# Optimization experiments

Measured on AMD Instinct MI355X. Metric: run time of the kernel, lower is better.

## Reference

```python
import jax, jax.numpy as jnp
import numpy as np

N, D, E, K = 16384, 512, 8, 2  # tokens, model dim, experts, top_k


def setup_inputs() -> dict:
    key = jax.random.key(0)
    k_x, k_l, k_w = jax.random.split(key, 3)
    input_batch = jax.random.normal(k_x, (N, D), dtype=jnp.float32)
    # Router-like top-k gates: distinct expert ids per token (matches the
    # module's assumption that each (token, slot) maps to a unique expert row).
    logits = jax.random.normal(k_l, (N, E), dtype=jnp.float32)
    top_vals, top_idx = jax.lax.top_k(logits, K)
    probabilities = jax.nn.softmax(top_vals, axis=-1)          # [N, K]
    indices = top_idx.astype(jnp.int32)                        # [N, K]
    W = jax.random.normal(k_w, (E, D, D), dtype=jnp.float32) * (1.0 / np.sqrt(D))
    b = jnp.zeros((E, D), dtype=jnp.float32)
    return {"input_batch": input_batch, "probabilities": probabilities,
            "indices": indices, "W": W, "b": b}


def reference(input_batch, probabilities, indices, W, b):
    # Original loops over experts, gathers tokens routed to each expert,
    # runs the expert, concatenates, restores original (token, slot) order,
    # applies AFTER_EXPERTS gate weighting, and sums over the top_k slots.
    # Equivalent vectorized math: out[n] = sum_k p[n,k] * expert_{idx[n,k]}(x[n]).
    y = jnp.einsum('nd,edo->eno', input_batch, W) + b[:, None, :]   # [E, N, D]
    n_ar = jnp.arange(input_batch.shape[0])[:, None]                # [N, 1]
    gathered = y[indices, n_ar]                                     # [N, K, D]
    output = jnp.sum(probabilities[..., None] * gathered, axis=1)   # [N, D]
    total_loss = jnp.float32(0.0)  # sampler_loss=0 (external indices), expert losses=0
    return output, total_loss
```

## Files before the change

kernel.cpp:

```cpp
#include <hip/hip_runtime.h>

#define NTOK 16384
#define DIM  512
#define NEXP 8
#define NPAIR 64
#define PCAP 8192

#define BM 128
#define BN 64
#define BK 32

typedef __bf16 bf16x8 __attribute__((ext_vector_type(8)));
typedef __bf16 bf16x4 __attribute__((ext_vector_type(4)));
typedef float  f32x4  __attribute__((ext_vector_type(4)));

__device__ __forceinline__ void async_cp16(const void* g, void* l) {
    __builtin_amdgcn_global_load_lds((const __attribute__((address_space(1))) void*)g,
                                     (__attribute__((address_space(3))) void*)l, 16, 0, 0);
}

__global__ __launch_bounds__(256) void k_prep(const float* __restrict__ W,
                                              __bf16* __restrict__ Wt,
                                              const float* __restrict__ x,
                                              __bf16* __restrict__ xb,
                                              const int* __restrict__ indices,
                                              const float* __restrict__ probs,
                                              int* __restrict__ cnt,
                                              int* __restrict__ tok_arr,
                                              float* __restrict__ plo_arr,
                                              float* __restrict__ phi_arr,
                                              float* __restrict__ out) {
    int b = blockIdx.x, tid = threadIdx.x;
    if (b < 2048) {
        __shared__ __bf16 tile[32][34];
        int e = b >> 8, rem = b & 255;
        int o0 = (rem >> 4) * 32, k0 = (rem & 15) * 32;
        const float* Wsrc = W + ((size_t)e * DIM + k0) * DIM + o0;
        for (int i = tid; i < 1024; i += 256) {
            int kk = i >> 5, oo = i & 31;
            tile[oo][kk] = (__bf16)Wsrc[(size_t)kk * DIM + oo];
        }
        __syncthreads();
        __bf16* dst = Wt + ((size_t)(e * 16 + (k0 >> 5)) * DIM + o0) * 32;
        for (int i = tid; i < 1024; i += 256) {
            int oo = i >> 5, kk = i & 31;
            dst[oo * 32 + kk] = tile[oo][kk];
        }
    } else if (b < 2304) {
        int base = (b - 2048) * 256 + tid;
        const float4* src = (const float4*)x;
        #pragma unroll
        for (int it = 0; it < 32; ++it) {
            int i = base + it * 65536;
            float4 v = src[i];
            bf16x4 h; h[0] = (__bf16)v.x; h[1] = (__bf16)v.y; h[2] = (__bf16)v.z; h[3] = (__bf16)v.w;
            *(bf16x4*)&xb[(size_t)i * 4] = h;
        }
    } else {
        __shared__ int lcnt[NPAIR], lbase[NPAIR];
        int t = (b - 2304) * 256 + tid;
        if (tid < NPAIR) lcnt[tid] = 0;
        __syncthreads();
        int   e0 = indices[2 * t], e1 = indices[2 * t + 1];
        float p0 = probs[2 * t],   p1 = probs[2 * t + 1];
        int lo = min(e0, e1), hi = max(e0, e1);
        float plo = (e0 < e1) ? p0 : p1;
        float phi = (e0 < e1) ? p1 : p0;
        int key = lo * 8 + hi;
        int lr = atomicAdd(&lcnt[key], 1);
        __syncthreads();
        if (tid < NPAIR) lbase[tid] = atomicAdd(&cnt[tid], lcnt[tid]);
        __syncthreads();
        int pos = lbase[key] + lr;
        if (pos < PCAP) {
            int q = key * PCAP + pos;
            tok_arr[q] = t; plo_arr[q] = plo; phi_arr[q] = phi;
        }
        if (b == 2304 && tid == 0) out[NTOK * DIM] = 0.0f;
    }
}

__global__ __launch_bounds__(256) void k_gemm(const __bf16* __restrict__ xb,
                                              const __bf16* __restrict__ Wt,
                                              const float* __restrict__ bias,
                                              const int* __restrict__ tok_arr,
                                              const float* __restrict__ plo_arr,
                                              const float* __restrict__ phi_arr,
                                              const int* __restrict__ cnt,
                                              float* __restrict__ out) {
    int p = blockIdx.x;
    int r = p & 7;
    int nt = (p >> 3) & 7;
    int m_slot = (p >> 6) * 8 + r;
    int key = -1, m_t = 0, count = 0, total = 0;
    for (int i = 0; i < NPAIR; ++i) {
        int c = cnt[i];
        int tl = (c + BM - 1) >> 7;
        if (key < 0 && m_slot < total + tl) { key = i; m_t = m_slot - total; count = c; }
        total += tl;
    }
    if (key < 0) return;
    if (count > PCAP) count = PCAP;
    int lo = key >> 3, hi = key & 7;
    int m0 = m_t * BM, n0 = nt * BN, tid = threadIdx.x;

    __shared__ __attribute__((aligned(16))) char smem[32768];
    __shared__ int   sTok[BM];
    __shared__ float sPlo[BM], sPhi[BM];

    if (tid < BM) {
        int g = m0 + tid;
        int tk = 0; float a = 0.f, h = 0.f;
        if (g < count) {
            int q = key * PCAP + g;
            tk = tok_arr[q]; a = plo_arr[q]; h = phi_arr[q];
        }
        sTok[tid] = tk;
        sPlo[tid] = a; sPhi[tid] = h;
    }
    __syncthreads();

    int wid  = tid >> 6, lane = tid & 63;
    int quad = lane >> 4, rr  = lane & 15;
    int wm = (wid >> 1) * 64, wn = (wid & 1) * 32;

    int rA0 = tid >> 2;
    int swz = ((tid & 3) ^ (rA0 & 3)) << 3;
    const __bf16* gA0 = xb + (size_t)sTok[rA0]      * DIM + swz;
    const __bf16* gA1 = xb + (size_t)sTok[rA0 + 64] * DIM + swz;
    size_t bOff = (size_t)((rA0 * 4 + ((tid & 3) ^ (rA0 & 3))) * 8);
    const __bf16* gBlo = Wt + ((size_t)(lo * 16) * DIM + n0) * 32 + bOff;
    const __bf16* gBhi = Wt + ((size_t)(hi * 16) * DIM + n0) * 32 + bOff;

    f32x4 accL[4][2] = {};
    f32x4 accH[4][2] = {};

    async_cp16(gA0,  smem + tid * 16);
    async_cp16(gA1,  smem + tid * 16 + 4096);
    async_cp16(gBlo, smem + 16384 + tid * 16);
    async_cp16(gBhi, smem + 24576 + tid * 16);

    #pragma unroll 2
    for (int kt = 0; kt < 16; ++kt) {
        int cur = kt & 1;
        __syncthreads();
        if (kt < 15) {
            int ka = (kt + 1) * BK;
            size_t wOff = (size_t)(kt + 1) * DIM * 32;
            int nx = (kt + 1) & 1;
            async_cp16(gA0 + ka,    smem + nx * 8192 + tid * 16);
            async_cp16(gA1 + ka,    smem + nx * 8192 + tid * 16 + 4096);
            async_cp16(gBlo + wOff, smem + 16384 + nx * 4096 + tid * 16);
            async_cp16(gBhi + wOff, smem + 24576 + nx * 4096 + tid * 16);
        }
        const __bf16* sA  = (const __bf16*)(smem +         cur * 8192);
        const __bf16* sBl = (const __bf16*)(smem + 16384 + cur * 4096);
        const __bf16* sBh = (const __bf16*)(smem + 24576 + cur * 4096);
        int csw = (quad ^ (rr & 3)) * 8;
        bf16x8 af[4], bl[2], bh[2];
        #pragma unroll
        for (int i = 0; i < 4; ++i)
            af[i] = *(bf16x8*)&sA[(wm + i * 16 + rr) * BK + csw];
        #pragma unroll
        for (int j = 0; j < 2; ++j) {
            bl[j] = *(bf16x8*)&sBl[(wn + j * 16 + rr) * BK + csw];
            bh[j] = *(bf16x8*)&sBh[(wn + j * 16 + rr) * BK + csw];
        }
        #pragma unroll
        for (int i = 0; i < 4; ++i)
            #pragma unroll
            for (int j = 0; j < 2; ++j) {
                accL[i][j] = __builtin_amdgcn_mfma_f32_16x16x32_bf16(af[i], bl[j], accL[i][j], 0, 0, 0);
                accH[i][j] = __builtin_amdgcn_mfma_f32_16x16x32_bf16(af[i], bh[j], accH[i][j], 0, 0, 0);
            }
    }

    float blo[2], bhi[2];
    #pragma unroll
    for (int j = 0; j < 2; ++j) {
        blo[j] = bias[lo * DIM + n0 + wn + j * 16 + rr];
        bhi[j] = bias[hi * DIM + n0 + wn + j * 16 + rr];
    }
    #pragma unroll
    for (int i = 0; i < 4; ++i) {
        #pragma unroll
        for (int reg = 0; reg < 4; ++reg) {
            int row = wm + i * 16 + quad * 4 + reg;
            int g = m0 + row;
            if (g >= count) continue;
            int   tk = sTok[row];
            float pl = sPlo[row], ph = sPhi[row];
            float* dst = out + (size_t)tk * DIM + n0 + wn + rr;
            #pragma unroll
            for (int j = 0; j < 2; ++j)
                dst[j * 16] = accL[i][j][reg] * pl + accH[i][j][reg] * ph + pl * blo[j] + ph * bhi[j];
        }
    }
}

extern "C" void kernel_launch(void* const* d_in, const int* in_sizes, int n_in,
                              void* d_out, int out_size, void* d_ws, size_t ws_size,
                              hipStream_t stream) {
    const float* x    = (const float*)d_in[0];
    const float* prob = (const float*)d_in[1];
    const int*   idx  = (const int*)d_in[2];
    const float* W    = (const float*)d_in[3];
    const float* b    = (const float*)d_in[4];
    float* out = (float*)d_out;

    char* ws = (char*)d_ws;
    __bf16* Wt      = (__bf16*)ws;
    __bf16* xb      = (__bf16*)(ws + 4194304);
    int*    cnt     = (int*)   (ws + 4194304 + 16777216);
    int*    tok_arr = (int*)   (ws + 4194304 + 16777216 + 256);
    float*  plo_arr = (float*) (ws + 4194304 + 16777216 + 256 + 2097152);
    float*  phi_arr = (float*) (ws + 4194304 + 16777216 + 256 + 2 * 2097152);

    (void)hipMemsetAsync(cnt, 0, NPAIR * sizeof(int), stream);
    hipLaunchKernelGGL(k_prep, dim3(2368), dim3(256), 0, stream,
                       W, Wt, x, xb, idx, prob, cnt, tok_arr, plo_arr, phi_arr, out);
    hipLaunchKernelGGL(k_gemm, dim3(1280), dim3(256), 0, stream,
                       xb, Wt, b, tok_arr, plo_arr, phi_arr, cnt, out);
}
```

Before: 138.1 us.

## Triple-buffer GEMM LDS with explicit vmcnt waits and MFMA priority

Switches the grouped expert GEMM from double to triple buffering in LDS, so loads are issued two k-steps ahead. The combined syncthreads is replaced by explicit s_waitcnt vmcnt plus s_barrier, and the loop is fully unrolled. The MFMA block is wrapped in s_setprio, and launch bounds ask for 3 blocks per CU. The goal is to hide global-load latency behind compute, at the cost of 48KB LDS per block, which may limit occupancy, and of fragile manual vmcnt accounting.

Measured after the change: 137.4 us. No clear change (-0.5%).

```diff
diff --git a/kernel.cpp b/kernel.cpp
--- a/kernel.cpp
+++ b/kernel.cpp
@@ -80,14 +80,14 @@
     }
 }
 
-__global__ __launch_bounds__(256) void k_gemm(const __bf16* __restrict__ xb,
-                                              const __bf16* __restrict__ Wt,
-                                              const float* __restrict__ bias,
-                                              const int* __restrict__ tok_arr,
-                                              const float* __restrict__ plo_arr,
-                                              const float* __restrict__ phi_arr,
-                                              const int* __restrict__ cnt,
-                                              float* __restrict__ out) {
+__global__ __launch_bounds__(256, 3) void k_gemm(const __bf16* __restrict__ xb,
+                                                 const __bf16* __restrict__ Wt,
+                                                 const float* __restrict__ bias,
+                                                 const int* __restrict__ tok_arr,
+                                                 const float* __restrict__ plo_arr,
+                                                 const float* __restrict__ phi_arr,
+                                                 const int* __restrict__ cnt,
+                                                 float* __restrict__ out) {
     int p = blockIdx.x;
     int r = p & 7;
     int nt = (p >> 3) & 7;
@@ -104,7 +104,7 @@
     int lo = key >> 3, hi = key & 7;
     int m0 = m_t * BM, n0 = nt * BN, tid = threadIdx.x;
 
-    __shared__ __attribute__((aligned(16))) char smem[32768];
+    __shared__ __attribute__((aligned(16))) char smem[49152];
     __shared__ int   sTok[BM];
     __shared__ float sPlo[BM], sPhi[BM];
 
@@ -135,27 +135,30 @@
     f32x4 accL[4][2] = {};
     f32x4 accH[4][2] = {};
 
-    async_cp16(gA0,  smem + tid * 16);
-    async_cp16(gA1,  smem + tid * 16 + 4096);
-    async_cp16(gBlo, smem + 16384 + tid * 16);
-    async_cp16(gBhi, smem + 24576 + tid * 16);
-
-    #pragma unroll 2
+    auto issue = [&](int kt, int b) {
+        int ka = kt * BK;
+        size_t wOff = (size_t)kt * DIM * 32;
+        async_cp16(gA0 + ka,    smem + b * 8192 + tid * 16);
+        async_cp16(gA1 + ka,    smem + b * 8192 + tid * 16 + 4096);
+        async_cp16(gBlo + wOff, smem + 24576 + b * 4096 + tid * 16);
+        async_cp16(gBhi + wOff, smem + 36864 + b * 4096 + tid * 16);
+    };
+
+    issue(0, 0);
+    issue(1, 1);
+
+    int cur = 0;
+    #pragma unroll
     for (int kt = 0; kt < 16; ++kt) {
-        int cur = kt & 1;
-        __syncthreads();
-        if (kt < 15) {
-            int ka = (kt + 1) * BK;
-            size_t wOff = (size_t)(kt + 1) * DIM * 32;
-            int nx = (kt + 1) & 1;
-            async_cp16(gA0 + ka,    smem + nx * 8192 + tid * 16);
-            async_cp16(gA1 + ka,    smem + nx * 8192 + tid * 16 + 4096);
-            async_cp16(gBlo + wOff, smem + 16384 + nx * 4096 + tid * 16);
-            async_cp16(gBhi + wOff, smem + 24576 + nx * 4096 + tid * 16);
-        }
+        if (kt < 15) { asm volatile("s_waitcnt vmcnt(4)" ::: "memory"); }
+        else         { asm volatile("s_waitcnt vmcnt(0)" ::: "memory"); }
+        __builtin_amdgcn_s_barrier();
+        asm volatile("" ::: "memory");
+        if (kt < 14) issue(kt + 2, cur == 0 ? 2 : cur - 1);
+
         const __bf16* sA  = (const __bf16*)(smem +         cur * 8192);
-        const __bf16* sBl = (const __bf16*)(smem + 16384 + cur * 4096);
-        const __bf16* sBh = (const __bf16*)(smem + 24576 + cur * 4096);
+        const __bf16* sBl = (const __bf16*)(smem + 24576 + cur * 4096);
+        const __bf16* sBh = (const __bf16*)(smem + 36864 + cur * 4096);
         int csw = (quad ^ (rr & 3)) * 8;
         bf16x8 af[4], bl[2], bh[2];
         #pragma unroll
@@ -166,6 +169,7 @@
             bl[j] = *(bf16x8*)&sBl[(wn + j * 16 + rr) * BK + csw];
             bh[j] = *(bf16x8*)&sBh[(wn + j * 16 + rr) * BK + csw];
         }
+        __builtin_amdgcn_s_setprio(1);
         #pragma unroll
         for (int i = 0; i < 4; ++i)
             #pragma unroll
@@ -173,6 +177,8 @@
                 accL[i][j] = __builtin_amdgcn_mfma_f32_16x16x32_bf16(af[i], bl[j], accL[i][j], 0, 0, 0);
                 accH[i][j] = __builtin_amdgcn_mfma_f32_16x16x32_bf16(af[i], bh[j], accH[i][j], 0, 0, 0);
             }
+        __builtin_amdgcn_s_setprio(0);
+        cur = (cur == 2) ? 0 : cur + 1;
     }
 
     float blo[2], bhi[2];
```
